# Kernel tuning notes

Measured on AMD Instinct MI355X. Metric: run time of the kernel, lower is better.

Reference implementation:

```python
import jax, jax.numpy as jnp
import numpy as np

B, C_HIGH, C_LOW, H, W = 4, 256, 128, 64, 64
HEADS = 4
HEAD_DIM = C_LOW // HEADS
FFN = 2 * C_LOW
EPS = 1e-5


def group_norm1(x, w, b):
    # GroupNorm(num_groups=1): normalize over (C,H,W) per sample, per-channel affine
    mu = jnp.mean(x, axis=(1, 2, 3), keepdims=True)
    var = jnp.var(x, axis=(1, 2, 3), keepdims=True)
    xn = (x - mu) * jax.lax.rsqrt(var + EPS)
    return xn * w[None, :, None, None] + b[None, :, None, None]


def conv1x1(x, Wm):
    # 1x1 conv, no bias: Wm [C_out, C_in], x [B,C_in,H,W]
    return jnp.einsum('oc,bchw->bohw', Wm, x)


def setup_inputs() -> dict:
    key = jax.random.key(0)
    ks = jax.random.split(key, 10)
    s = 0.05
    return {
        'high_feature': jax.random.normal(ks[0], (B, C_HIGH, H, W), jnp.float32),
        'low_feature': jax.random.normal(ks[1], (B, C_LOW, H, W), jnp.float32),
        'norm_high_w': jnp.ones((C_HIGH,), jnp.float32),
        'norm_high_b': jnp.zeros((C_HIGH,), jnp.float32),
        'norm_low_w': jnp.ones((C_LOW,), jnp.float32),
        'norm_low_b': jnp.zeros((C_LOW,), jnp.float32),
        'norm_ffn_w': jnp.ones((C_LOW,), jnp.float32),
        'norm_ffn_b': jnp.zeros((C_LOW,), jnp.float32),
        'Wq': jax.random.normal(ks[2], (C_LOW, C_HIGH), jnp.float32) * s,
        'Wk': jax.random.normal(ks[3], (C_LOW, C_LOW), jnp.float32) * s,
        'Wv': jax.random.normal(ks[4], (C_LOW, C_LOW), jnp.float32) * s,
        'Wproj': jax.random.normal(ks[5], (C_LOW, C_LOW), jnp.float32) * s,
        'Wffn1': jax.random.normal(ks[6], (FFN, C_LOW), jnp.float32) * s,
        'Wffn2': jax.random.normal(ks[7], (C_LOW, FFN), jnp.float32) * s,
        # nn.Parameter(torch.zeros(1)) in the original; use 0.1 for nontrivial grads
        'gamma_attn': jnp.full((1,), 0.1, jnp.float32),
        'gamma_ffn': jnp.full((1,), 0.1, jnp.float32),
    }


def reference(high_feature, low_feature, norm_high_w, norm_high_b, norm_low_w,
              norm_low_b, norm_ffn_w, norm_ffn_b, Wq, Wk, Wv, Wproj, Wffn1,
              Wffn2, gamma_attn, gamma_ffn):
    Bb, _, Hh, Ww = low_feature.shape
    N = Hh * Ww
    scale = HEAD_DIM ** (-0.5)

    high_norm = group_norm1(high_feature, norm_high_w, norm_high_b)
    low_norm = group_norm1(low_feature, norm_low_w, norm_low_b)

    q = conv1x1(high_norm, Wq).reshape(Bb, HEADS, HEAD_DIM, N).transpose(0, 1, 3, 2)  # [B,h,N,d]
    k = conv1x1(low_norm, Wk).reshape(Bb, HEADS, HEAD_DIM, N)                         # [B,h,d,N]
    v = conv1x1(low_norm, Wv).reshape(Bb, HEADS, HEAD_DIM, N).transpose(0, 1, 3, 2)   # [B,h,N,d]

    attn = jax.nn.softmax(jnp.einsum('bhnd,bhdm->bhnm', q, k) * scale, axis=-1)       # [B,h,N,N]
    out = jnp.einsum('bhnm,bhmd->bhnd', attn, v)                                      # [B,h,N,d]
    out = out.transpose(0, 1, 3, 2).reshape(Bb, C_LOW, Hh, Ww)
    out = conv1x1(out, Wproj)

    x = low_feature + gamma_attn[0] * out
    xn = group_norm1(x, norm_ffn_w, norm_ffn_b)
    ffn = conv1x1(jax.nn.gelu(conv1x1(xn, Wffn1), approximate=False), Wffn2)
    return x + gamma_ffn[0] * ffn
```

## Files before the change

### kernel.cpp

```cpp
#include <hip/hip_runtime.h>
#include <hip/hip_bf16.h>
#include <math.h>

#define EPS 1e-5f
#define BB 4
#define CHIGH 256
#define CLOW 128
#define NN 4096
#define NHEADS 4
#define HDIM 32
#define FFN_DIM 256
#define SPLITS 4

typedef __bf16 b8 __attribute__((ext_vector_type(8)));
typedef float f4 __attribute__((ext_vector_type(4)));

__device__ __forceinline__ unsigned int cvt_pk(float lo, float hi) {
    float2 t; t.x = lo; t.y = hi;
    __hip_bfloat162 h = __float22bfloat162_rn(t);
    unsigned int r;
    __builtin_memcpy(&r, &h, sizeof(r));
    return r;
}
__device__ __forceinline__ float b2f(unsigned short u) {
    unsigned int x = ((unsigned int)u) << 16;
    float f;
    __builtin_memcpy(&f, &x, 4);
    return f;
}
__device__ __forceinline__ float fexp2(float x) {
#if __has_builtin(__builtin_amdgcn_exp2f)
    return __builtin_amdgcn_exp2f(x);
#else
    return exp2f(x);
#endif
}

__global__ __launch_bounds__(256)
void prep_kernel(const float* __restrict__ high, const float* __restrict__ low,
                 float* __restrict__ acc,
                 const float* __restrict__ w0, const float* __restrict__ w1,
                 const float* __restrict__ w2, const float* __restrict__ w3,
                 const float* __restrict__ w4, const float* __restrict__ w5,
                 unsigned short* __restrict__ dst)
{
    const int z = blockIdx.z;
    if (z < 2) {
        const int perSample = z == 0 ? CHIGH * NN : CLOW * NN;
        const float* X = z == 0 ? high : low;
        float* ac = acc + (z == 0 ? 0 : 8);
        const int b = blockIdx.y;
        const float4* xp = (const float4*)(X + (size_t)b * perSample);
        const int n4 = perSample >> 2;
        float s = 0.f, s2 = 0.f;
        for (int i = blockIdx.x * blockDim.x + threadIdx.x; i < n4;
             i += gridDim.x * blockDim.x) {
            float4 v = xp[i];
            s  += v.x + v.y + v.z + v.w;
            s2 += v.x * v.x + v.y * v.y + v.z * v.z + v.w * v.w;
        }
        for (int off = 32; off; off >>= 1) {
            s  += __shfl_down(s, off, 64);
            s2 += __shfl_down(s2, off, 64);
        }
        __shared__ float ls[4], ls2[4];
        const int w = threadIdx.x >> 6;
        if ((threadIdx.x & 63) == 0) { ls[w] = s; ls2[w] = s2; }
        __syncthreads();
        if (threadIdx.x == 0) {
            atomicAdd(&ac[2 * b], ls[0] + ls[1] + ls[2] + ls[3]);
            atomicAdd(&ac[2 * b + 1], ls2[0] + ls2[1] + ls2[2] + ls2[3]);
        }
    } else {
        const int idx = blockIdx.y * 64 + blockIdx.x;
        const int m = idx >> 5;
        if (m >= 6) return;
        const int sizes[6] = {32768, 16384, 16384, 16384, 32768, 32768};
        const int offs[6]  = {0, 32768, 49152, 65536, 81920, 114688};
        const int Ks[6]    = {256, 128, 128, 128, 128, 256};
        const float* src = m == 0 ? w0 : m == 1 ? w1 : m == 2 ? w2 : m == 3 ? w3
                         : m == 4 ? w4 : w5;
        const int i = ((idx & 31) * 256 + threadIdx.x) * 4;
        if (i >= sizes[m]) return;
        const int K = Ks[m];
        const int row = i / K, col = i % K;
        const int mt = row >> 4, mr = row & 15;
        const int kt = col >> 5, kr = col & 31;
        float4 v = *(const float4*)&src[i];
        uint2 pk;
        pk.x = cvt_pk(v.x, v.y);
        pk.y = cvt_pk(v.z, v.w);
        const int doff = offs[m] + (((mt * (K >> 5)) + kt) << 9) + (mr << 5) + kr;
        *(uint2*)&dst[doff] = pk;
    }
}

__global__ __launch_bounds__(256)
void qkv_kernel(const unsigned short* __restrict__ wbf,
                const float* __restrict__ high, const float* __restrict__ low,
                unsigned short* __restrict__ Qt, unsigned short* __restrict__ Kt,
                unsigned short* __restrict__ Vt,
                const float* __restrict__ nh_w, const float* __restrict__ nh_b,
                const float* __restrict__ nl_w, const float* __restrict__ nl_b,
                const float* __restrict__ st)
{
    __shared__ unsigned short XsRaw[32 * 264];
    const int b = blockIdx.y;
    const int n0 = blockIdx.x * 32;
    const int t = threadIdx.x;
    const int w = t >> 6, lm = t & 15, quad = (t & 63) >> 4;
    const int fo = lm * 32 + quad * 8;
    unsigned int* xw = (unsigned int*)XsRaw;

    if (blockIdx.z == 0) {
        const float invCnt = 1.0f / ((float)CHIGH * NN);
        const float mean = st[2 * b] * invCnt;
        const float rstd = rsqrtf(st[2 * b + 1] * invCnt - mean * mean + EPS);
        const float* Xb = high + (size_t)b * CHIGH * NN;
        #pragma unroll
        for (int it = 0; it < 4; it++) {
            const int s = it * 256 + t;
            const int kp = s >> 3;
            const int k2 = kp << 1;
            const int nc = (s & 7) << 2;
            const size_t ro = (size_t)k2 * NN + n0 + nc;
            float4 pa = *(const float4*)&Xb[ro];
            float4 pb = *(const float4*)&Xb[ro + NN];
            const float sc0 = nh_w[k2] * rstd,     sb0 = nh_b[k2] - mean * sc0;
            const float sc1 = nh_w[k2 + 1] * rstd, sb1 = nh_b[k2 + 1] - mean * sc1;
            pa.x = pa.x * sc0 + sb0; pa.y = pa.y * sc0 + sb0;
            pa.z = pa.z * sc0 + sb0; pa.w = pa.w * sc0 + sb0;
            pb.x = pb.x * sc1 + sb1; pb.y = pb.y * sc1 + sb1;
            pb.z = pb.z * sc1 + sb1; pb.w = pb.w * sc1 + sb1;
            xw[(nc + 0) * 132 + kp] = cvt_pk(pa.x, pb.x);
            xw[(nc + 1) * 132 + kp] = cvt_pk(pa.y, pb.y);
            xw[(nc + 2) * 132 + kp] = cvt_pk(pa.z, pb.z);
            xw[(nc + 3) * 132 + kp] = cvt_pk(pa.w, pb.w);
        }
        __syncthreads();
        const int ng = w & 1, mh = w >> 1;
        f4 acc[4];
        #pragma unroll
        for (int f = 0; f < 4; f++) acc[f] = (f4){0.f, 0.f, 0.f, 0.f};
        #pragma unroll
        for (int kc = 0; kc < 8; kc++) {
            b8 bx = *(const b8*)&XsRaw[(ng * 16 + lm) * 264 + kc * 32 + quad * 8];
            #pragma unroll
            for (int f = 0; f < 4; f++) {
                b8 af = *(const b8*)&wbf[(((mh * 4 + f) * 8 + kc) << 9) + fo];
                acc[f] = __builtin_amdgcn_mfma_f32_16x16x32_bf16(af, bx, acc[f], 0, 0, 0);
            }
        }
        const int n = n0 + ng * 16 + lm;
        const float oscale = 0.25503480f;
        #pragma unroll
        for (int f = 0; f < 4; f++) {
            const int mb = mh * 64 + f * 16 + quad * 4;
            const int hh = mb >> 5, ddb = mb & 31;
            uint2 pk;
            pk.x = cvt_pk(acc[f][0] * oscale, acc[f][1] * oscale);
            pk.y = cvt_pk(acc[f][2] * oscale, acc[f][3] * oscale);
            *(uint2*)&Qt[((size_t)(b * NHEADS + hh) * NN + n) * 32 + ddb] = pk;
        }
    } else {
        const unsigned short* Wb = wbf + 32768;
        const float invCnt = 1.0f / ((float)CLOW * NN);
        const float mean = st[8 + 2 * b] * invCnt;
        const float rstd = rsqrtf(st[8 + 2 * b + 1] * invCnt - mean * mean + EPS);
        const float* Xb = low + (size_t)b * CLOW * NN;
        #pragma unroll
        for (int it = 0; it < 2; it++) {
            const int s = it * 256 + t;
            const int kp = s >> 3;
            const int k2 = kp << 1;
            const int nc = (s & 7) << 2;
            const size_t ro = (size_t)k2 * NN + n0 + nc;
            float4 pa = *(const float4*)&Xb[ro];
            float4 pb = *(const float4*)&Xb[ro + NN];
            const float sc0 = nl_w[k2] * rstd,     sb0 = nl_b[k2] - mean * sc0;
            const float sc1 = nl_w[k2 + 1] * rstd, sb1 = nl_b[k2 + 1] - mean * sc1;
            pa.x = pa.x * sc0 + sb0; pa.y = pa.y * sc0 + sb0;
            pa.z = pa.z * sc0 + sb0; pa.w = pa.w * sc0 + sb0;
            pb.x = pb.x * sc1 + sb1; pb.y = pb.y * sc1 + sb1;
            pb.z = pb.z * sc1 + sb1; pb.w = pb.w * sc1 + sb1;
            xw[(nc + 0) * 68 + kp] = cvt_pk(pa.x, pb.x);
            xw[(nc + 1) * 68 + kp] = cvt_pk(pa.y, pb.y);
            xw[(nc + 2) * 68 + kp] = cvt_pk(pa.z, pb.z);
            xw[(nc + 3) * 68 + kp] = cvt_pk(pa.w, pb.w);
        }
        __syncthreads();
        f4 acc[2][4];
        #pragma unroll
        for (int ng = 0; ng < 2; ng++)
            #pragma unroll
            for (int f = 0; f < 4; f++) acc[ng][f] = (f4){0.f, 0.f, 0.f, 0.f};
        #pragma unroll
        for (int kc = 0; kc < 4; kc++) {
            b8 bx0 = *(const b8*)&XsRaw[lm * 136 + kc * 32 + quad * 8];
            b8 bx1 = *(const b8*)&XsRaw[(16 + lm) * 136 + kc * 32 + quad * 8];
            #pragma unroll
            for (int f = 0; f < 4; f++) {
                b8 af = *(const b8*)&Wb[(((w * 4 + f) * 4 + kc) << 9) + fo];
                acc[0][f] = __builtin_amdgcn_mfma_f32_16x16x32_bf16(af, bx0, acc[0][f], 0, 0, 0);
                acc[1][f] = __builtin_amdgcn_mfma_f32_16x16x32_bf16(af, bx1, acc[1][f], 0, 0, 0);
            }
        }
        if (w < 2) {
            #pragma unroll
            for (int ng = 0; ng < 2; ng++) {
                const int n = n0 + ng * 16 + lm;
                #pragma unroll
                for (int f = 0; f < 4; f++) {
                    const int mb = w * 64 + f * 16 + quad * 4;
                    const int hh = mb >> 5, ddb = mb & 31;
                    uint2 pk;
                    pk.x = cvt_pk(acc[ng][f][0], acc[ng][f][1]);
                    pk.y = cvt_pk(acc[ng][f][2], acc[ng][f][3]);
                    *(uint2*)&Kt[((size_t)(b * NHEADS + hh) * NN + n) * 32 + ddb] = pk;
                }
            }
        } else {
            #pragma unroll
            for (int ng = 0; ng < 2; ng++) {
                const int n = n0 + ng * 16 + lm;
                const size_t nblk = ((size_t)(n >> 5) << 10) + (n & 31);
                #pragma unroll
                for (int f = 0; f < 4; f++) {
                    const int db = (w - 2) * 64 + f * 16 + quad * 4;
                    const int hh = db >> 5;
                    const size_t hb = (size_t)(b * NHEADS + hh) * NN * 32;
                    #pragma unroll
                    for (int r = 0; r < 4; r++) {
                        const int d = (db + r) & 31;
                        unsigned int u = cvt_pk(acc[ng][f][r], 0.f);
                        Vt[hb + nblk + (size_t)d * 32] = (unsigned short)(u & 0xFFFF);
                    }
                }
            }
        }
    }
}

__global__ __launch_bounds__(512)
void flash_kernel(const unsigned short* __restrict__ Qt,
                  const unsigned short* __restrict__ Kt,
                  const unsigned short* __restrict__ Vt,
                  unsigned short* __restrict__ Op, float* __restrict__ Lp)
{
    __shared__ unsigned short Ps[8][32][72];

    const int lid = blockIdx.x;
    const int xcd = lid & 7, slot = lid >> 3;
    const int g = xcd * 8 + (slot >> 4);
    const int xblk = slot & 15;
    const int half = g >> 4, bh = g & 15;
    const int b = bh >> 2, h = bh & 3;
    const int n0 = xblk * 256;
    const int t = threadIdx.x;
    const int w = t >> 6;
    const int lm = t & 15, quad = (t & 63) >> 4;

    const unsigned short* Qh = Qt + (size_t)(b * NHEADS + h) * NN * 32;
    const unsigned short* Kh = Kt + (size_t)(b * NHEADS + h) * NN * 32;
    const unsigned short* Vh = Vt + (size_t)(b * NHEADS + h) * NN * 32;

    b8 aq[2];
    aq[0] = *(const b8*)&Qh[(size_t)(n0 + w * 32 + lm) * 32 + quad * 8];
    aq[1] = *(const b8*)&Qh[(size_t)(n0 + w * 32 + 16 + lm) * 32 + quad * 8];

    b8 ones;
    #pragma unroll
    for (int j = 0; j < 8; j++) ones[j] = (__bf16)1.0f;

    f4 ocT[2][2];
    f4 lsum[2];
    #pragma unroll
    for (int u = 0; u < 2; u++) {
        lsum[u] = (f4){0.f, 0.f, 0.f, 0.f};
        ocT[0][u] = (f4){0.f, 0.f, 0.f, 0.f};
        ocT[1][u] = (f4){0.f, 0.f, 0.f, 0.f};
    }

    const int m_lo = half * (NN / SPLITS), m_hi = m_lo + NN / SPLITS;
    for (int m0 = m_lo; m0 < m_hi; m0 += 64) {
        b8 bk[4], av[2][2];
        #pragma unroll
        for (int f = 0; f < 4; f++)
            bk[f] = *(const b8*)&Kh[(size_t)(m0 + f * 16 + lm) * 32 + quad * 8];
        #pragma unroll
        for (int c = 0; c < 2; c++) {
            const size_t vb = (size_t)(m0 + c * 32) * 32 + quad * 8;
            av[0][c] = *(const b8*)&Vh[vb + (size_t)lm * 32];
            av[1][c] = *(const b8*)&Vh[vb + (size_t)(16 + lm) * 32];
        }

        f4 st[4][2];
        #pragma unroll
        for (int f = 0; f < 4; f++)
            #pragma unroll
            for (int u = 0; u < 2; u++) {
                f4 z = {0.f, 0.f, 0.f, 0.f};
                st[f][u] = __builtin_amdgcn_mfma_f32_16x16x32_bf16(bk[f], aq[u], z, 0, 0, 0);
            }

        #pragma unroll
        for (int f = 0; f < 4; f++)
            #pragma unroll
            for (int u = 0; u < 2; u++) {
                uint2 pk;
                pk.x = cvt_pk(fexp2(st[f][u][0]), fexp2(st[f][u][1]));
                pk.y = cvt_pk(fexp2(st[f][u][2]), fexp2(st[f][u][3]));
                *(uint2*)&Ps[w][u * 16 + lm][f * 16 + quad * 4] = pk;
            }

        #pragma unroll
        for (int c = 0; c < 2; c++)
            #pragma unroll
            for (int u = 0; u < 2; u++) {
                b8 bp = *(const b8*)&Ps[w][u * 16 + lm][c * 32 + quad * 8];
                ocT[0][u] = __builtin_amdgcn_mfma_f32_16x16x32_bf16(av[0][c], bp, ocT[0][u], 0, 0, 0);
                ocT[1][u] = __builtin_amdgcn_mfma_f32_16x16x32_bf16(av[1][c], bp, ocT[1][u], 0, 0, 0);
                lsum[u]   = __builtin_amdgcn_mfma_f32_16x16x32_bf16(ones, bp, lsum[u], 0, 0, 0);
            }
    }

    unsigned short* OpB = Op + ((size_t)(half * BB + b) * CLOW + h * HDIM) * NN;
    float* LpB = Lp + ((size_t)(half * BB + b) * NHEADS + h) * NN;
    #pragma unroll
    for (int u = 0; u < 2; u++) {
        const int n = n0 + w * 32 + u * 16 + lm;
        if (quad == 0) LpB[n] = lsum[u][0];
        #pragma unroll
        for (int hh = 0; hh < 2; hh++)
            #pragma unroll
            for (int r = 0; r < 4; r++) {
                const int d = hh * 16 + quad * 4 + r;
                unsigned int uu = cvt_pk(ocT[hh][u][r], 0.f);
                OpB[(size_t)d * NN + n] = (unsigned short)(uu & 0xFFFF);
            }
    }
}

__global__ __launch_bounds__(256)
void proj_kernel(const unsigned short* __restrict__ Wb,
                 const unsigned short* __restrict__ Opart, const float* __restrict__ Lp,
                 const float* __restrict__ low, float* __restrict__ Xout,
                 const float* __restrict__ gp, float* __restrict__ stOut)
{
    __shared__ unsigned short Xs[32][136];
    __shared__ float red[8];
    const int b = blockIdx.z;
    const int mblk = blockIdx.y;
    const int n0 = blockIdx.x * 32;
    const int t = threadIdx.x;
    const int w = t >> 6, lm = t & 15, quad = (t & 63) >> 4;
    const int ng = w & 1, mh = w >> 1;
    const int fo = lm * 32 + quad * 8;
    unsigned int* xw = (unsigned int*)&Xs[0][0];

    #pragma unroll
    for (int it = 0; it < 2; it++) {
        const int s = it * 256 + t;
        const int kp = s >> 3;
        const int k2 = kp << 1;
        const int nc = (s & 7) << 2;
        const size_t ro = (size_t)k2 * NN + n0 + nc;
        const int hh = k2 >> 5;
        const size_t lo = (size_t)(b * NHEADS + hh) * NN + n0 + nc;
        float4 l4 = *(const float4*)&Lp[lo];
        #pragma unroll
        for (int sp = 1; sp < SPLITS; sp++)
            l4 += *(const float4*)&Lp[lo + (size_t)sp * BB * NHEADS * NN];
        float4 pa = {0.f, 0.f, 0.f, 0.f}, pb = {0.f, 0.f, 0.f, 0.f};
        #pragma unroll
        for (int sp = 0; sp < SPLITS; sp++) {
            const unsigned short* Os = Opart + (size_t)sp * BB * CLOW * NN
                                     + (size_t)b * CLOW * NN + ro;
            ushort4 ua = *(const ushort4*)Os;
            ushort4 ub = *(const ushort4*)(Os + NN);
            pa.x += b2f(ua.x); pa.y += b2f(ua.y); pa.z += b2f(ua.z); pa.w += b2f(ua.w);
            pb.x += b2f(ub.x); pb.y += b2f(ub.y); pb.z += b2f(ub.z); pb.w += b2f(ub.w);
        }
        float4 iv;
        iv.x = 1.f / l4.x; iv.y = 1.f / l4.y; iv.z = 1.f / l4.z; iv.w = 1.f / l4.w;
        pa.x *= iv.x; pa.y *= iv.y; pa.z *= iv.z; pa.w *= iv.w;
        pb.x *= iv.x; pb.y *= iv.y; pb.z *= iv.z; pb.w *= iv.w;
        xw[(nc + 0) * 68 + kp] = cvt_pk(pa.x, pb.x);
        xw[(nc + 1) * 68 + kp] = cvt_pk(pa.y, pb.y);
        xw[(nc + 2) * 68 + kp] = cvt_pk(pa.z, pb.z);
        xw[(nc + 3) * 68 + kp] = cvt_pk(pa.w, pb.w);
    }
    __syncthreads();

    f4 acc[2];
    acc[0] = (f4){0.f, 0.f, 0.f, 0.f};
    acc[1] = (f4){0.f, 0.f, 0.f, 0.f};
    #pragma unroll
    for (int kc = 0; kc < 4; kc++) {
        b8 bx = *(const b8*)&Xs[ng * 16 + lm][kc * 32 + quad * 8];
        #pragma unroll
        for (int f = 0; f < 2; f++) {
            const int mt = mblk * 4 + mh * 2 + f;
            b8 af = *(const b8*)&Wb[((mt * 4 + kc) << 9) + fo];
            acc[f] = __builtin_amdgcn_mfma_f32_16x16x32_bf16(af, bx, acc[f], 0, 0, 0);
        }
    }

    const float g = gp[0];
    const float* Rb = low + (size_t)b * CLOW * NN;
    float* Yb = Xout + (size_t)b * CLOW * NN;
    const int n = n0 + ng * 16 + lm;
    float s = 0.f, s2 = 0.f;
    #pragma unroll
    for (int f = 0; f < 2; f++)
        #pragma unroll
        for (int r = 0; r < 4; r++) {
            const int m = mblk * 64 + mh * 32 + f * 16 + quad * 4 + r;
            const size_t off = (size_t)m * NN + n;
            float v = Rb[off] + g * acc[f][r];
            Yb[off] = v;
            s += v; s2 += v * v;
        }
    for (int off = 32; off; off >>= 1) {
        s  += __shfl_down(s, off, 64);
        s2 += __shfl_down(s2, off, 64);
    }
    if ((t & 63) == 0) { red[w] = s; red[4 + w] = s2; }
    __syncthreads();
    if (t == 0) {
        atomicAdd(&stOut[2 * b], red[0] + red[1] + red[2] + red[3]);
        atomicAdd(&stOut[2 * b + 1], red[4] + red[5] + red[6] + red[7]);
    }
}

__global__ __launch_bounds__(512)
void ffn_kernel(const unsigned short* __restrict__ W1, const unsigned short* __restrict__ W2,
                const float* __restrict__ X, float* __restrict__ Out,
                const float* __restrict__ nw, const float* __restrict__ nb,
                const float* __restrict__ st, const float* __restrict__ gp)
{
    __shared__ unsigned short Xs[32][136];
    __shared__ unsigned short Hs[32][264];
    const int b = blockIdx.y;
    const int n0 = blockIdx.x * 32;
    const int t = threadIdx.x;
    const int w = t >> 6, lm = t & 15, quad = (t & 63) >> 4;
    const int fo = lm * 32 + quad * 8;

    const float invCnt = 1.0f / ((float)CLOW * NN);
    const float mean = st[2 * b] * invCnt;
    const float rstd = rsqrtf(st[2 * b + 1] * invCnt - mean * mean + EPS);

    const float* Xb = X + (size_t)b * CLOW * NN;
    unsigned int* xw = (unsigned int*)&Xs[0][0];
    {
        const int s = t;
        const int kp = s >> 3;
        const int k2 = kp << 1;
        const int nc = (s & 7) << 2;
        const size_t ro = (size_t)k2 * NN + n0 + nc;
        float4 pa = *(const float4*)&Xb[ro];
        float4 pb = *(const float4*)&Xb[ro + NN];
        const float sc0 = nw[k2] * rstd,     sb0 = nb[k2] - mean * sc0;
        const float sc1 = nw[k2 + 1] * rstd, sb1 = nb[k2 + 1] - mean * sc1;
        pa.x = pa.x * sc0 + sb0; pa.y = pa.y * sc0 + sb0;
        pa.z = pa.z * sc0 + sb0; pa.w = pa.w * sc0 + sb0;
        pb.x = pb.x * sc1 + sb1; pb.y = pb.y * sc1 + sb1;
        pb.z = pb.z * sc1 + sb1; pb.w = pb.w * sc1 + sb1;
        xw[(nc + 0) * 68 + kp] = cvt_pk(pa.x, pb.x);
        xw[(nc + 1) * 68 + kp] = cvt_pk(pa.y, pb.y);
        xw[(nc + 2) * 68 + kp] = cvt_pk(pa.z, pb.z);
        xw[(nc + 3) * 68 + kp] = cvt_pk(pa.w, pb.w);
    }
    __syncthreads();

    f4 hv[2][2];
    #pragma unroll
    for (int ng = 0; ng < 2; ng++) {
        hv[ng][0] = (f4){0.f, 0.f, 0.f, 0.f};
        hv[ng][1] = (f4){0.f, 0.f, 0.f, 0.f};
    }
    #pragma unroll
    for (int kc = 0; kc < 4; kc++) {
        b8 bx0 = *(const b8*)&Xs[lm][kc * 32 + quad * 8];
        b8 bx1 = *(const b8*)&Xs[16 + lm][kc * 32 + quad * 8];
        #pragma unroll
        for (int f = 0; f < 2; f++) {
            const int mt = w * 2 + f;
            b8 af = *(const b8*)&W1[((mt * 4 + kc) << 9) + fo];
            hv[0][f] = __builtin_amdgcn_mfma_f32_16x16x32_bf16(af, bx0, hv[0][f], 0, 0, 0);
            hv[1][f] = __builtin_amdgcn_mfma_f32_16x16x32_bf16(af, bx1, hv[1][f], 0, 0, 0);
        }
    }
    #pragma unroll
    for (int ng = 0; ng < 2; ng++)
        #pragma unroll
        for (int f = 0; f < 2; f++) {
            float g0 = hv[ng][f][0], g1 = hv[ng][f][1];
            float g2 = hv[ng][f][2], g3 = hv[ng][f][3];
            g0 = 0.5f * g0 * (1.f + erff(g0 * 0.70710678118654752f));
            g1 = 0.5f * g1 * (1.f + erff(g1 * 0.70710678118654752f));
            g2 = 0.5f * g2 * (1.f + erff(g2 * 0.70710678118654752f));
            g3 = 0.5f * g3 * (1.f + erff(g3 * 0.70710678118654752f));
            uint2 pk;
            pk.x = cvt_pk(g0, g1);
            pk.y = cvt_pk(g2, g3);
            *(uint2*)&Hs[ng * 16 + lm][w * 32 + f * 16 + quad * 4] = pk;
        }
    __syncthreads();

    f4 o[2];
    o[0] = (f4){0.f, 0.f, 0.f, 0.f};
    o[1] = (f4){0.f, 0.f, 0.f, 0.f};
    #pragma unroll
    for (int kc = 0; kc < 8; kc++) {
        b8 bh0 = *(const b8*)&Hs[lm][kc * 32 + quad * 8];
        b8 bh1 = *(const b8*)&Hs[16 + lm][kc * 32 + quad * 8];
        b8 af = *(const b8*)&W2[((w * 8 + kc) << 9) + fo];
        o[0] = __builtin_amdgcn_mfma_f32_16x16x32_bf16(af, bh0, o[0], 0, 0, 0);
        o[1] = __builtin_amdgcn_mfma_f32_16x16x32_bf16(af, bh1, o[1], 0, 0, 0);
    }
    const float g = gp[0];
    float* Ob = Out + (size_t)b * CLOW * NN;
    #pragma unroll
    for (int ng = 0; ng < 2; ng++) {
        const int n = n0 + ng * 16 + lm;
        #pragma unroll
        for (int r = 0; r < 4; r++) {
            const int m = w * 16 + quad * 4 + r;
            const size_t off = (size_t)m * NN + n;
            Ob[off] = Xb[off] + g * o[ng][r];
        }
    }
}

extern "C" void kernel_launch(void* const* d_in, const int* in_sizes, int n_in,
                              void* d_out, int out_size, void* d_ws, size_t ws_size,
                              hipStream_t stream)
{
    const float* high  = (const float*)d_in[0];
    const float* low   = (const float*)d_in[1];
    const float* nh_w  = (const float*)d_in[2];
    const float* nh_b  = (const float*)d_in[3];
    const float* nl_w  = (const float*)d_in[4];
    const float* nl_b  = (const float*)d_in[5];
    const float* nf_w  = (const float*)d_in[6];
    const float* nf_b  = (const float*)d_in[7];
    const float* Wq    = (const float*)d_in[8];
    const float* Wk    = (const float*)d_in[9];
    const float* Wv    = (const float*)d_in[10];
    const float* Wproj = (const float*)d_in[11];
    const float* Wff1  = (const float*)d_in[12];
    const float* Wff2  = (const float*)d_in[13];
    const float* g_at  = (const float*)d_in[14];
    const float* g_ff  = (const float*)d_in[15];
    float* out = (float*)d_out;

    float* ws    = (float*)d_ws;
    float* stats = ws;
    unsigned short* wbf = (unsigned short*)(ws + 64);
    unsigned short* qt = wbf + 147456;
    unsigned short* kt = qt + (size_t)BB * NHEADS * NN * 32;
    unsigned short* vt = kt + (size_t)BB * NHEADS * NN * 32;
    unsigned short* opart = vt + (size_t)BB * CLOW * NN;
    float* lpart = (float*)(opart + (size_t)SPLITS * BB * CLOW * NN);
    float* x     = lpart + (size_t)SPLITS * BB * NHEADS * NN;

    (void)hipMemsetAsync(stats, 0, 64 * sizeof(float), stream);

    prep_kernel<<<dim3(64, BB, 3), 256, 0, stream>>>(high, low, stats,
                                                     Wq, Wk, Wv, Wproj, Wff1, Wff2, wbf);

    qkv_kernel<<<dim3(128, BB, 2), 256, 0, stream>>>(wbf, high, low, qt, kt, vt,
                                                     nh_w, nh_b, nl_w, nl_b, stats);

    flash_kernel<<<dim3(1024), 512, 0, stream>>>(qt, kt, vt, opart, lpart);

    proj_kernel<<<dim3(128, 2, BB), 256, 0, stream>>>(wbf + 65536, opart, lpart,
                                                      low, x, g_at, stats + 16);

    ffn_kernel<<<dim3(128, BB), 512, 0, stream>>>(wbf + 81920, wbf + 114688, x, out,
                                                  nf_w, nf_b, stats + 16, g_ff);
}
```

Before: 229.7 us.

## Software-pipeline K loads in flash loop and merge proj output blocks

The flash attention loop now double-buffers K fragments so the next tile's K loads are issued before the current tile's MFMAs, and the kernel gets an occupancy hint in its launch bounds. The proj kernel drops its output-channel split: each block now computes all 128 output channels for 32 positions, which halves the grid and avoids normalizing the attention partials twice. The stats reduction loop is unrolled by two with independent accumulators, and the qkv loads are batched ahead of the math to raise memory-level parallelism. Costs are higher register pressure and fewer proj blocks, so occupancy and parallelism may drop.

```diff
diff --git a/kernel.cpp b/kernel.cpp
--- a/kernel.cpp
+++ b/kernel.cpp
@@ -52,13 +52,23 @@
         const int b = blockIdx.y;
         const float4* xp = (const float4*)(X + (size_t)b * perSample);
         const int n4 = perSample >> 2;
-        float s = 0.f, s2 = 0.f;
-        for (int i = blockIdx.x * blockDim.x + threadIdx.x; i < n4;
-             i += gridDim.x * blockDim.x) {
+        const int stride = gridDim.x * blockDim.x;
+        int i = blockIdx.x * blockDim.x + threadIdx.x;
+        float s = 0.f, s2 = 0.f, sB = 0.f, s2B = 0.f;
+        for (; i + stride < n4; i += 2 * stride) {
+            float4 v = xp[i];
+            float4 u = xp[i + stride];
+            s  += v.x + v.y + v.z + v.w;
+            s2 += v.x * v.x + v.y * v.y + v.z * v.z + v.w * v.w;
+            sB  += u.x + u.y + u.z + u.w;
+            s2B += u.x * u.x + u.y * u.y + u.z * u.z + u.w * u.w;
+        }
+        if (i < n4) {
             float4 v = xp[i];
             s  += v.x + v.y + v.z + v.w;
             s2 += v.x * v.x + v.y * v.y + v.z * v.z + v.w * v.w;
         }
+        s += sB; s2 += s2B;
         for (int off = 32; off; off >>= 1) {
             s  += __shfl_down(s, off, 64);
             s2 += __shfl_down(s2, off, 64);
@@ -117,6 +127,8 @@
         const float mean = st[2 * b] * invCnt;
         const float rstd = rsqrtf(st[2 * b + 1] * invCnt - mean * mean + EPS);
         const float* Xb = high + (size_t)b * CHIGH * NN;
+        float4 ra[4], rb[4];
+        float wa[4], wb_[4], ca[4], cb[4];
         #pragma unroll
         for (int it = 0; it < 4; it++) {
             const int s = it * 256 + t;
@@ -124,10 +136,19 @@
             const int k2 = kp << 1;
             const int nc = (s & 7) << 2;
             const size_t ro = (size_t)k2 * NN + n0 + nc;
-            float4 pa = *(const float4*)&Xb[ro];
-            float4 pb = *(const float4*)&Xb[ro + NN];
-            const float sc0 = nh_w[k2] * rstd,     sb0 = nh_b[k2] - mean * sc0;
-            const float sc1 = nh_w[k2 + 1] * rstd, sb1 = nh_b[k2 + 1] - mean * sc1;
+            ra[it] = *(const float4*)&Xb[ro];
+            rb[it] = *(const float4*)&Xb[ro + NN];
+            wa[it] = nh_w[k2]; wb_[it] = nh_w[k2 + 1];
+            ca[it] = nh_b[k2]; cb[it] = nh_b[k2 + 1];
+        }
+        #pragma unroll
+        for (int it = 0; it < 4; it++) {
+            const int s = it * 256 + t;
+            const int kp = s >> 3;
+            const int nc = (s & 7) << 2;
+            float4 pa = ra[it], pb = rb[it];
+            const float sc0 = wa[it] * rstd,  sb0 = ca[it] - mean * sc0;
+            const float sc1 = wb_[it] * rstd, sb1 = cb[it] - mean * sc1;
             pa.x = pa.x * sc0 + sb0; pa.y = pa.y * sc0 + sb0;
             pa.z = pa.z * sc0 + sb0; pa.w = pa.w * sc0 + sb0;
             pb.x = pb.x * sc1 + sb1; pb.y = pb.y * sc1 + sb1;
@@ -168,6 +189,8 @@
         const float mean = st[8 + 2 * b] * invCnt;
         const float rstd = rsqrtf(st[8 + 2 * b + 1] * invCnt - mean * mean + EPS);
         const float* Xb = low + (size_t)b * CLOW * NN;
+        float4 ra[2], rb[2];
+        float wa[2], wb_[2], ca[2], cb[2];
         #pragma unroll
         for (int it = 0; it < 2; it++) {
             const int s = it * 256 + t;
@@ -175,10 +198,19 @@
             const int k2 = kp << 1;
             const int nc = (s & 7) << 2;
             const size_t ro = (size_t)k2 * NN + n0 + nc;
-            float4 pa = *(const float4*)&Xb[ro];
-            float4 pb = *(const float4*)&Xb[ro + NN];
-            const float sc0 = nl_w[k2] * rstd,     sb0 = nl_b[k2] - mean * sc0;
-            const float sc1 = nl_w[k2 + 1] * rstd, sb1 = nl_b[k2 + 1] - mean * sc1;
+            ra[it] = *(const float4*)&Xb[ro];
+            rb[it] = *(const float4*)&Xb[ro + NN];
+            wa[it] = nl_w[k2]; wb_[it] = nl_w[k2 + 1];
+            ca[it] = nl_b[k2]; cb[it] = nl_b[k2 + 1];
+        }
+        #pragma unroll
+        for (int it = 0; it < 2; it++) {
+            const int s = it * 256 + t;
+            const int kp = s >> 3;
+            const int nc = (s & 7) << 2;
+            float4 pa = ra[it], pb = rb[it];
+            const float sc0 = wa[it] * rstd,  sb0 = ca[it] - mean * sc0;
+            const float sc1 = wb_[it] * rstd, sb1 = cb[it] - mean * sc1;
             pa.x = pa.x * sc0 + sb0; pa.y = pa.y * sc0 + sb0;
             pa.z = pa.z * sc0 + sb0; pa.w = pa.w * sc0 + sb0;
             pb.x = pb.x * sc1 + sb1; pb.y = pb.y * sc1 + sb1;
@@ -241,7 +273,7 @@
     }
 }
 
-__global__ __launch_bounds__(512)
+__global__ __launch_bounds__(512, 8)
 void flash_kernel(const unsigned short* __restrict__ Qt,
                   const unsigned short* __restrict__ Kt,
                   const unsigned short* __restrict__ Vt,
@@ -281,38 +313,30 @@
         ocT[1][u] = (f4){0.f, 0.f, 0.f, 0.f};
     }
 
-    const int m_lo = half * (NN / SPLITS), m_hi = m_lo + NN / SPLITS;
-    for (int m0 = m_lo; m0 < m_hi; m0 += 64) {
-        b8 bk[4], av[2][2];
+    auto loadK = [&](int m0, b8* bk) {
         #pragma unroll
         for (int f = 0; f < 4; f++)
             bk[f] = *(const b8*)&Kh[(size_t)(m0 + f * 16 + lm) * 32 + quad * 8];
+    };
+    auto tile = [&](int m0, const b8* bk) {
+        b8 av[2][2];
         #pragma unroll
         for (int c = 0; c < 2; c++) {
             const size_t vb = (size_t)(m0 + c * 32) * 32 + quad * 8;
             av[0][c] = *(const b8*)&Vh[vb + (size_t)lm * 32];
             av[1][c] = *(const b8*)&Vh[vb + (size_t)(16 + lm) * 32];
         }
-
-        f4 st[4][2];
         #pragma unroll
         for (int f = 0; f < 4; f++)
             #pragma unroll
             for (int u = 0; u < 2; u++) {
                 f4 z = {0.f, 0.f, 0.f, 0.f};
-                st[f][u] = __builtin_amdgcn_mfma_f32_16x16x32_bf16(bk[f], aq[u], z, 0, 0, 0);
-            }
-
-        #pragma unroll
-        for (int f = 0; f < 4; f++)
-            #pragma unroll
-            for (int u = 0; u < 2; u++) {
+                f4 sv = __builtin_amdgcn_mfma_f32_16x16x32_bf16(bk[f], aq[u], z, 0, 0, 0);
                 uint2 pk;
-                pk.x = cvt_pk(fexp2(st[f][u][0]), fexp2(st[f][u][1]));
-                pk.y = cvt_pk(fexp2(st[f][u][2]), fexp2(st[f][u][3]));
+                pk.x = cvt_pk(fexp2(sv[0]), fexp2(sv[1]));
+                pk.y = cvt_pk(fexp2(sv[2]), fexp2(sv[3]));
                 *(uint2*)&Ps[w][u * 16 + lm][f * 16 + quad * 4] = pk;
             }
-
         #pragma unroll
         for (int c = 0; c < 2; c++)
             #pragma unroll
@@ -322,6 +346,18 @@
                 ocT[1][u] = __builtin_amdgcn_mfma_f32_16x16x32_bf16(av[1][c], bp, ocT[1][u], 0, 0, 0);
                 lsum[u]   = __builtin_amdgcn_mfma_f32_16x16x32_bf16(ones, bp, lsum[u], 0, 0, 0);
             }
+    };
+
+    const int m_lo = half * (NN / SPLITS);
+    constexpr int nT = NN / SPLITS / 64;
+    b8 bkA[4], bkB[4];
+    loadK(m_lo, bkA);
+    for (int it = 0; it < nT; it += 2) {
+        loadK(m_lo + (it + 1) * 64, bkB);
+        tile(m_lo + it * 64, bkA);
+        const int m2 = (it + 2 < nT) ? m_lo + (it + 2) * 64 : m_lo;
+        loadK(m2, bkA);
+        tile(m_lo + (it + 1) * 64, bkB);
     }
 
     unsigned short* OpB = Op + ((size_t)(half * BB + b) * CLOW + h * HDIM) * NN;
@@ -349,12 +385,10 @@
 {
     __shared__ unsigned short Xs[32][136];
     __shared__ float red[8];
-    const int b = blockIdx.z;
-    const int mblk = blockIdx.y;
+    const int b = blockIdx.y;
     const int n0 = blockIdx.x * 32;
     const int t = threadIdx.x;
     const int w = t >> 6, lm = t & 15, quad = (t & 63) >> 4;
-    const int ng = w & 1, mh = w >> 1;
     const int fo = lm * 32 + quad * 8;
     unsigned int* xw = (unsigned int*)&Xs[0][0];
 
@@ -392,34 +426,42 @@
     }
     __syncthreads();
 
-    f4 acc[2];
-    acc[0] = (f4){0.f, 0.f, 0.f, 0.f};
-    acc[1] = (f4){0.f, 0.f, 0.f, 0.f};
+    f4 acc[2][2];
+    #pragma unroll
+    for (int f = 0; f < 2; f++) {
+        acc[f][0] = (f4){0.f, 0.f, 0.f, 0.f};
+        acc[f][1] = (f4){0.f, 0.f, 0.f, 0.f};
+    }
     #pragma unroll
     for (int kc = 0; kc < 4; kc++) {
-        b8 bx = *(const b8*)&Xs[ng * 16 + lm][kc * 32 + quad * 8];
+        b8 bx0 = *(const b8*)&Xs[lm][kc * 32 + quad * 8];
+        b8 bx1 = *(const b8*)&Xs[16 + lm][kc * 32 + quad * 8];
         #pragma unroll
         for (int f = 0; f < 2; f++) {
-            const int mt = mblk * 4 + mh * 2 + f;
+            const int mt = w * 2 + f;
             b8 af = *(const b8*)&Wb[((mt * 4 + kc) << 9) + fo];
-            acc[f] = __builtin_amdgcn_mfma_f32_16x16x32_bf16(af, bx, acc[f], 0, 0, 0);
+            acc[f][0] = __builtin_amdgcn_mfma_f32_16x16x32_bf16(af, bx0, acc[f][0], 0, 0, 0);
+            acc[f][1] = __builtin_amdgcn_mfma_f32_16x16x32_bf16(af, bx1, acc[f][1], 0, 0, 0);
         }
     }
 
     const float g = gp[0];
     const float* Rb = low + (size_t)b * CLOW * NN;
     float* Yb = Xout + (size_t)b * CLOW * NN;
-    const int n = n0 + ng * 16 + lm;
     float s = 0.f, s2 = 0.f;
     #pragma unroll
     for (int f = 0; f < 2; f++)
         #pragma unroll
-        for (int r = 0; r < 4; r++) {
-            const int m = mblk * 64 + mh * 32 + f * 16 + quad * 4 + r;
-            const size_t off = (size_t)m * NN + n;
-            float v = Rb[off] + g * acc[f][r];
-            Yb[off] = v;
-            s += v; s2 += v * v;
+        for (int ng = 0; ng < 2; ng++) {
+            const int n = n0 + ng * 16 + lm;
+            #pragma unroll
+            for (int r = 0; r < 4; r++) {
+                const int m = w * 32 + f * 16 + quad * 4 + r;
+                const size_t off = (size_t)m * NN + n;
+                float v = Rb[off] + g * acc[f][ng][r];
+                Yb[off] = v;
+                s += v; s2 += v * v;
+            }
         }
     for (int off = 32; off; off >>= 1) {
         s  += __shfl_down(s, off, 64);
@@ -576,8 +618,8 @@
 
     flash_kernel<<<dim3(1024), 512, 0, stream>>>(qt, kt, vt, opart, lpart);
 
-    proj_kernel<<<dim3(128, 2, BB), 256, 0, stream>>>(wbf + 65536, opart, lpart,
-                                                      low, x, g_at, stats + 16);
+    proj_kernel<<<dim3(128, BB), 256, 0, stream>>>(wbf + 65536, opart, lpart,
+                                                   low, x, g_at, stats + 16);
 
     ffn_kernel<<<dim3(128, BB), 512, 0, stream>>>(wbf + 81920, wbf + 114688, x, out,
                                                   nf_w, nf_b, stats + 16, g_ff);
```

Result: slower. 325.6 us (+41.7%).
